# Optimization experiments

Hardware: AMD Instinct MI355X
Metric: run time of the kernel (lower is better)

## Reference

```python
import jax, jax.numpy as jnp
import numpy as np

N = 50000      # total nodes across batch of graphs
E = 800000     # total directed edges (avg degree 16)
B = 64         # number of graphs
D = 128        # input_dim == hidden_dim
L = 4          # num_layers - 1 GIN layers
OUT = 10
BN_EPS = 1e-5


def setup_inputs() -> dict:
    key = jax.random.key(0)
    ks = jax.random.split(key, 12)
    s = 0.05
    return {
        "x": jax.random.normal(ks[0], (N, D), jnp.float32),
        "pi": jax.random.uniform(ks[1], (B, 25), jnp.float32),
        "eps": jnp.zeros((L,), jnp.float32),
        "mlp_w1": jax.random.normal(ks[2], (L, D, D), jnp.float32) * s,
        "mlp_b1": jnp.zeros((L, D), jnp.float32),
        "mlp_bn_g": jnp.ones((L, D), jnp.float32),
        "mlp_bn_b": jnp.zeros((L, D), jnp.float32),
        "mlp_w2": jax.random.normal(ks[3], (L, D, D), jnp.float32) * s,
        "mlp_b2": jnp.zeros((L, D), jnp.float32),
        "bn_g": jnp.ones((L, D), jnp.float32),
        "bn_b": jnp.zeros((L, D), jnp.float32),
        "attend_w": jax.random.normal(ks[4], (D * (L + 1), 1), jnp.float32) * s,
        "attend_b": jnp.zeros((1,), jnp.float32),
        "pi_w": jax.random.normal(ks[5], (25, 16), jnp.float32) * s,
        "pi_b": jnp.zeros((16,), jnp.float32),
        "out_w": jax.random.normal(ks[6], (D * (L + 1) + 16, OUT), jnp.float32) * s,
        "out_b": jnp.zeros((OUT,), jnp.float32),
        "edge_index": jax.random.randint(ks[7], (2, E), 0, N, dtype=jnp.int32),
        "graph_id": jnp.sort(jax.random.randint(ks[8], (N,), 0, B, dtype=jnp.int32)),
    }


def _bn(z, g, b):
    # BatchNorm1d in training mode over all nodes (axis 0)
    m = z.mean(axis=0)
    v = z.var(axis=0)
    return (z - m) * jax.lax.rsqrt(v + BN_EPS) * g + b


def reference(x, pi, eps, mlp_w1, mlp_b1, mlp_bn_g, mlp_bn_b, mlp_w2, mlp_b2,
              bn_g, bn_b, attend_w, attend_b, pi_w, pi_b, out_w, out_b,
              edge_index, graph_id):
    src, dst = edge_index[0], edge_index[1]
    h = x
    reps = [x]
    for l in range(L):
        # GIN sum aggregation (learn_eps=True: no self-loops in Adj)
        pooled = jax.ops.segment_sum(h[src], dst, num_segments=N)
        pooled = pooled + (1.0 + eps[l]) * h
        # 2-layer MLP: Linear -> BN -> ReLU -> Linear
        z = jax.nn.relu(_bn(pooled @ mlp_w1[l] + mlp_b1[l], mlp_bn_g[l], mlp_bn_b[l]))
        z = z @ mlp_w2[l] + mlp_b2[l]
        # outer BN + ReLU
        h = jax.nn.relu(_bn(z, bn_g[l], bn_b[l]))
        reps.append(h)
    hr = jnp.concatenate(reps, axis=1)               # [N, D*(L+1)]
    # per-graph attention softmax over nodes
    scores = (hr @ attend_w + attend_b)[:, 0]        # [N]
    smax = jax.ops.segment_max(scores, graph_id, num_segments=B)
    e = jnp.exp(scores - smax[graph_id])
    denom = jax.ops.segment_sum(e, graph_id, num_segments=B)
    coef = e / denom[graph_id]
    gemb = jax.ops.segment_sum(hr * coef[:, None], graph_id, num_segments=B)  # [B, D*(L+1)]
    # persistence-image branch (PI computed host-side; treated as input)
    pie = jax.nn.relu(pi @ pi_w + pi_b)              # [B, 16]
    feat = jnp.concatenate([gemb, pie], axis=1)      # [B, D*(L+1)+16]
    return feat @ out_w + out_b                      # [B, OUT]
```

## Files before the change

### kernel.cpp

```cpp
#include <hip/hip_runtime.h>
#include <hip/hip_bf16.h>

#define NN 50000
#define EE 800000
#define BBG 64
#define DD 128
#define LLAY 4
#define HRW 640
#define NOUT 10
#define SCANB 196

typedef __hip_bfloat16 bf16;
typedef __attribute__((ext_vector_type(8))) short short8;
typedef __attribute__((ext_vector_type(4))) float f32x4;

__device__ __forceinline__ float b2f(bf16 v) { return __bfloat162float(v); }
__device__ __forceinline__ float bflo(unsigned u) { return __uint_as_float(u << 16); }
__device__ __forceinline__ float bfhi(unsigned u) { return __uint_as_float(u & 0xffff0000u); }
__device__ __forceinline__ unsigned short f2bs(float v) {
  bf16 h = __float2bfloat16(v);
  unsigned short r; __builtin_memcpy(&r, &h, 2); return r;
}
__device__ __forceinline__ int dtype_of(const void* __restrict__ bng) {
  return (*(const unsigned*)bng == 0x3F800000u) ? 1 : 0;
}
__device__ __forceinline__ float ldf(const void* __restrict__ p, long i, int dt) {
  return dt ? ((const float*)p)[i] : b2f(((const bf16*)p)[i]);
}

__device__ __forceinline__ int lower_bound_i(const int* __restrict__ a, int n, int key) {
  int lo = 0, hi = n;
  while (lo < hi) { int mid = (lo + hi) >> 1; if (a[mid] < key) lo = mid + 1; else hi = mid; }
  return lo;
}

__global__ __launch_bounds__(256) void gnn_init(const void* __restrict__ x,
                                                bf16* __restrict__ hrb,
                                                const void* __restrict__ w1,
                                                const void* __restrict__ w2,
                                                bf16* __restrict__ w1t,
                                                bf16* __restrict__ w2t,
                                                const void* __restrict__ aw,
                                                float* __restrict__ scores,
                                                const int* __restrict__ ei,
                                                int* __restrict__ counts,
                                                int* __restrict__ rel,
                                                const void* __restrict__ bng) {
  int dt = dtype_of(bng);
  int tid = threadIdx.x;
  if (blockIdx.x >= 6250) {
    int i = (blockIdx.x - 6250) * 256 + tid;
    int l = i >> 14, rem = i & 16383, n = rem >> 7, k = rem & 127;
    long src = (long)l * 16384 + k * 128 + n;
    w1t[i] = __float2bfloat16(ldf(w1, src, dt));
    w2t[i] = __float2bfloat16(ldf(w2, src, dt));
    return;
  }
  if (blockIdx.x >= 3125) {
    int e = (blockIdx.x - 3125) * 256 + tid;
    rel[e] = atomicAdd(&counts[ei[EE + e]], 1);
    return;
  }
  int n = blockIdx.x * 16 + (tid >> 4);
  int il = tid & 15;
  long base = (long)n * DD + il * 8;
  float v[8];
  if (dt) {
    float4 a0 = *(const float4*)((const float*)x + base);
    float4 a1 = *(const float4*)((const float*)x + base + 4);
    v[0] = a0.x; v[1] = a0.y; v[2] = a0.z; v[3] = a0.w;
    v[4] = a1.x; v[5] = a1.y; v[6] = a1.z; v[7] = a1.w;
  } else {
    uint4 u = *(const uint4*)((const bf16*)x + base);
    v[0] = bflo(u.x); v[1] = bfhi(u.x); v[2] = bflo(u.y); v[3] = bfhi(u.y);
    v[4] = bflo(u.z); v[5] = bfhi(u.z); v[6] = bflo(u.w); v[7] = bfhi(u.w);
  }
  uint4 o;
  o.x = (unsigned)f2bs(v[0]) | ((unsigned)f2bs(v[1]) << 16);
  o.y = (unsigned)f2bs(v[2]) | ((unsigned)f2bs(v[3]) << 16);
  o.z = (unsigned)f2bs(v[4]) | ((unsigned)f2bs(v[5]) << 16);
  o.w = (unsigned)f2bs(v[6]) | ((unsigned)f2bs(v[7]) << 16);
  *(uint4*)(hrb + (size_t)n * HRW + il * 8) = o;
  float ss = 0.f;
  #pragma unroll
  for (int k = 0; k < 8; k++) ss += v[k] * ldf(aw, il * 8 + k, dt);
  ss += __shfl_xor(ss, 1, 64); ss += __shfl_xor(ss, 2, 64);
  ss += __shfl_xor(ss, 4, 64); ss += __shfl_xor(ss, 8, 64);
  if (il == 0) unsafeAtomicAdd(&scores[n], ss);
}

__global__ __launch_bounds__(256) void gnn_scan1(const int* __restrict__ counts,
                                                 int* __restrict__ blocksum) {
  __shared__ int buf[256];
  int tid = threadIdx.x;
  int i = blockIdx.x * 256 + tid;
  buf[tid] = (i < NN) ? counts[i] : 0;
  __syncthreads();
  for (int s = 128; s > 0; s >>= 1) {
    if (tid < s) buf[tid] += buf[tid + s];
    __syncthreads();
  }
  if (tid == 0) blocksum[blockIdx.x] = buf[0];
}

__global__ __launch_bounds__(256) void gnn_scan3(const int* __restrict__ counts,
                                                 const int* __restrict__ blocksum,
                                                 int* __restrict__ rowstart) {
  __shared__ int buf[256];
  int tid = threadIdx.x;
  int partial = 0;
  for (int i = tid; i < blockIdx.x; i += 256) partial += blocksum[i];
  buf[tid] = partial;
  __syncthreads();
  for (int s = 128; s > 0; s >>= 1) {
    if (tid < s) buf[tid] += buf[tid + s];
    __syncthreads();
  }
  int offset = buf[0];
  __syncthreads();
  int i = blockIdx.x * 256 + tid;
  int v = (i < NN) ? counts[i] : 0;
  buf[tid] = v;
  __syncthreads();
  for (int ofs = 1; ofs < 256; ofs <<= 1) {
    int t = (tid >= ofs) ? buf[tid - ofs] : 0;
    __syncthreads();
    buf[tid] += t;
    __syncthreads();
  }
  int val = offset + buf[tid] - v;
  if (i < NN) rowstart[i] = val;
  if (blockIdx.x == SCANB - 1 && tid == 255) rowstart[NN] = offset + buf[255];
}

__global__ __launch_bounds__(256) void gnn_fill(const int* __restrict__ ei,
                                                const int* __restrict__ rowstart,
                                                const int* __restrict__ rel,
                                                int* __restrict__ csr_src) {
  int e = blockIdx.x * 256 + threadIdx.x;
  int src = ei[e];
  int dst = ei[EE + e];
  csr_src[rowstart[dst] + rel[e]] = src;
}

__device__ __forceinline__ void acc8(float* a, uint4 u) {
  a[0] += bflo(u.x); a[1] += bfhi(u.x);
  a[2] += bflo(u.y); a[3] += bfhi(u.y);
  a[4] += bflo(u.z); a[5] += bfhi(u.z);
  a[6] += bflo(u.w); a[7] += bfhi(u.w);
}

__device__ __forceinline__ float2 statsum(const float* __restrict__ stat, int c) {
  float s = 0.f, q = 0.f;
  #pragma unroll
  for (int k = 0; k < 8; k++) { s += stat[k * 256 + c]; q += stat[k * 256 + 128 + c]; }
  return make_float2(s, q);
}

__global__ __launch_bounds__(512) void gnn_gmg1(const bf16* __restrict__ hrb, int l,
                                                const int* __restrict__ rowstart,
                                                const int* __restrict__ csr_src,
                                                const void* __restrict__ eps,
                                                const bf16* __restrict__ Wt,
                                                const void* __restrict__ bias, int biasOfs,
                                                bf16* __restrict__ out,
                                                float* __restrict__ statOut,
                                                const void* __restrict__ bng) {
  int dt = dtype_of(bng);
  __shared__ __align__(16) unsigned ar[16][68];
  __shared__ int qhead;
  int tid = threadIdx.x, lane = tid & 63;
  int w = tid >> 6;
  int q = lane >> 4, il = lane & 15;
  int r0 = blockIdx.x * 16;
  const bf16* stripe = hrb + l * DD;
  float s = 1.0f + ldf(eps, l, dt);
  if (tid == 0) qhead = 0;
  __syncthreads();

  for (;;) {
    int i;
    if (lane == 0) i = atomicAdd(&qhead, 1);
    i = __shfl(i, 0, 64);
    if (i >= 16) break;
    int n = r0 + i;
    float a[8] = {0.f, 0.f, 0.f, 0.f, 0.f, 0.f, 0.f, 0.f};
    if (q == 0) {
      uint4 u = *(const uint4*)(stripe + (size_t)n * HRW + il * 8);
      a[0] = s * bflo(u.x); a[1] = s * bfhi(u.x);
      a[2] = s * bflo(u.y); a[3] = s * bfhi(u.y);
      a[4] = s * bflo(u.z); a[5] = s * bfhi(u.z);
      a[6] = s * bflo(u.w); a[7] = s * bfhi(u.w);
    }
    int start = rowstart[n], end = rowstart[n + 1];
    for (int base = start; base < end; base += 64) {
      int m = end - base; if (m > 64) m = 64;
      int idx = (base + lane < end) ? csr_src[base + lane] : 0;
      int j = 0;
      for (; j + 16 <= m; j += 16) {
        int s0 = __shfl(idx, j + q, 64);
        int s1 = __shfl(idx, j + 4 + q, 64);
        int s2 = __shfl(idx, j + 8 + q, 64);
        int s3 = __shfl(idx, j + 12 + q, 64);
        uint4 u0 = *(const uint4*)(stripe + (size_t)s0 * HRW + il * 8);
        uint4 u1 = *(const uint4*)(stripe + (size_t)s1 * HRW + il * 8);
        uint4 u2 = *(const uint4*)(stripe + (size_t)s2 * HRW + il * 8);
        uint4 u3 = *(const uint4*)(stripe + (size_t)s3 * HRW + il * 8);
        acc8(a, u0); acc8(a, u1); acc8(a, u2); acc8(a, u3);
      }
      for (; j + 8 <= m; j += 8) {
        int s0 = __shfl(idx, j + q, 64);
        int s1 = __shfl(idx, j + 4 + q, 64);
        uint4 u0 = *(const uint4*)(stripe + (size_t)s0 * HRW + il * 8);
        uint4 u1 = *(const uint4*)(stripe + (size_t)s1 * HRW + il * 8);
        acc8(a, u0); acc8(a, u1);
      }
      for (; j + 4 <= m; j += 4) {
        int src = __shfl(idx, j + q, 64);
        uint4 u = *(const uint4*)(stripe + (size_t)src * HRW + il * 8);
        acc8(a, u);
      }
      for (; j < m; j++) {
        int src = __shfl(idx, j, 64);
        if (q == 0) {
          uint4 u = *(const uint4*)(stripe + (size_t)src * HRW + il * 8);
          acc8(a, u);
        }
      }
    }
    #pragma unroll
    for (int k = 0; k < 8; k++) {
      a[k] += __shfl_xor(a[k], 16, 64);
      a[k] += __shfl_xor(a[k], 32, 64);
    }
    if (q == 0) {
      uint4 o;
      o.x = (unsigned)f2bs(a[0]) | ((unsigned)f2bs(a[1]) << 16);
      o.y = (unsigned)f2bs(a[2]) | ((unsigned)f2bs(a[3]) << 16);
      o.z = (unsigned)f2bs(a[4]) | ((unsigned)f2bs(a[5]) << 16);
      o.w = (unsigned)f2bs(a[6]) | ((unsigned)f2bs(a[7]) << 16);
      *(uint4*)&ar[i][il * 4] = o;
    }
  }
  __syncthreads();

  f32x4 acc = (f32x4){0.f, 0.f, 0.f, 0.f};
  #pragma unroll
  for (int ch = 0; ch < 4; ch++) {
    int k0 = ch * 32 + q * 8;
    uint4 raw = *(const uint4*)&ar[il][ch * 16 + q * 4];
    short8 af;
    __builtin_memcpy(&af, &raw, 16);
    short8 bfv = *(const short8*)(Wt + (w * 16 + il) * DD + k0);
    acc = __builtin_amdgcn_mfma_f32_16x16x32_bf16(af, bfv, acc, 0, 0, 0);
  }
  int col = w * 16 + il;
  float bv = ldf(bias, biasOfs + col, dt);
  float ss = 0.f, qq = 0.f;
  #pragma unroll
  for (int r = 0; r < 4; r++) {
    int row = r0 + q * 4 + r;
    float v = acc[r] + bv;
    out[(size_t)row * DD + col] = __float2bfloat16(v);
    ss += v; qq += v * v;
  }
  ss += __shfl_xor(ss, 16, 64);  ss += __shfl_xor(ss, 32, 64);
  qq += __shfl_xor(qq, 16, 64);  qq += __shfl_xor(qq, 32, 64);
  if (q == 0) {
    unsafeAtomicAdd(&statOut[(blockIdx.x & 7) * 256 + col], ss);
    unsafeAtomicAdd(&statOut[(blockIdx.x & 7) * 256 + 128 + col], qq);
  }
}

__global__ __launch_bounds__(256) void gnn_mgemm(const bf16* __restrict__ Abf,
                                                 const bf16* __restrict__ Wt,
                                                 const void* __restrict__ bias, int biasOfs,
                                                 bf16* __restrict__ out,
                                                 const float* __restrict__ statIn,
                                                 const void* __restrict__ g,
                                                 const void* __restrict__ bb, int parOfs,
                                                 float* __restrict__ statOut,
                                                 const void* __restrict__ bng) {
  int dt = dtype_of(bng);
  __shared__ float scf[128], shf[128];
  __shared__ float redS[4][128], redQ[4][128];
  int tid = threadIdx.x, w = tid >> 6, lane = tid & 63;
  int q = lane >> 4, il = lane & 15;
  if (tid < 128) {
    const float invN = 1.0f / NN;
    float2 sq = statsum(statIn, tid);
    float m = sq.x * invN;
    float rs = rsqrtf(sq.y * invN - m * m + 1e-5f);
    float gg = ldf(g, parOfs + tid, dt), bv = ldf(bb, parOfs + tid, dt);
    scf[tid] = rs * gg;
    shf[tid] = bv - m * rs * gg;
  }
  __syncthreads();
  int r0 = (blockIdx.x * 4 + w) * 16;
  int arow = r0 + il;
  int arowc = (arow < NN) ? arow : (NN - 1);
  f32x4 acc[8];
  #pragma unroll
  for (int i = 0; i < 8; i++) acc[i] = (f32x4){0.f, 0.f, 0.f, 0.f};
  #pragma unroll
  for (int ch = 0; ch < 4; ch++) {
    int k0 = ch * 32 + q * 8;
    uint4 raw = *(const uint4*)(Abf + (size_t)arowc * DD + k0);
    float4 c0 = *(const float4*)(scf + k0);
    float4 c1 = *(const float4*)(scf + k0 + 4);
    float4 d0 = *(const float4*)(shf + k0);
    float4 d1 = *(const float4*)(shf + k0 + 4);
    short8 af;
    af[0] = (short)f2bs(fmaxf(bflo(raw.x) * c0.x + d0.x, 0.f));
    af[1] = (short)f2bs(fmaxf(bfhi(raw.x) * c0.y + d0.y, 0.f));
    af[2] = (short)f2bs(fmaxf(bflo(raw.y) * c0.z + d0.z, 0.f));
    af[3] = (short)f2bs(fmaxf(bfhi(raw.y) * c0.w + d0.w, 0.f));
    af[4] = (short)f2bs(fmaxf(bflo(raw.z) * c1.x + d1.x, 0.f));
    af[5] = (short)f2bs(fmaxf(bfhi(raw.z) * c1.y + d1.y, 0.f));
    af[6] = (short)f2bs(fmaxf(bflo(raw.w) * c1.z + d1.z, 0.f));
    af[7] = (short)f2bs(fmaxf(bfhi(raw.w) * c1.w + d1.w, 0.f));
    #pragma unroll
    for (int ct = 0; ct < 8; ct++) {
      short8 bfv = *(const short8*)(Wt + (ct * 16 + il) * DD + k0);
      acc[ct] = __builtin_amdgcn_mfma_f32_16x16x32_bf16(af, bfv, acc[ct], 0, 0, 0);
    }
  }
  #pragma unroll
  for (int ct = 0; ct < 8; ct++) {
    int col = ct * 16 + il;
    float bv = ldf(bias, biasOfs + col, dt);
    float s = 0.f, qq = 0.f;
    #pragma unroll
    for (int r = 0; r < 4; r++) {
      int row = r0 + q * 4 + r;
      float v = acc[ct][r] + bv;
      if (row < NN) {
        out[(size_t)row * DD + col] = __float2bfloat16(v);
        s += v; qq += v * v;
      }
    }
    s += __shfl_xor(s, 16, 64);  s += __shfl_xor(s, 32, 64);
    qq += __shfl_xor(qq, 16, 64); qq += __shfl_xor(qq, 32, 64);
    if (q == 0) { redS[w][col] = s; redQ[w][col] = qq; }
  }
  __syncthreads();
  if (tid < 128) {
    float v = redS[0][tid] + redS[1][tid] + redS[2][tid] + redS[3][tid];
    unsafeAtomicAdd(&statOut[(blockIdx.x & 7) * 256 + tid], v);
  } else {
    int c = tid - 128;
    float v = redQ[0][c] + redQ[1][c] + redQ[2][c] + redQ[3][c];
    unsafeAtomicAdd(&statOut[(blockIdx.x & 7) * 256 + 128 + c], v);
  }
}

__global__ __launch_bounds__(256) void gnn_bn_relu(const bf16* __restrict__ z2,
                                                   const float* __restrict__ stat,
                                                   const void* __restrict__ g,
                                                   const void* __restrict__ bb, int parOfs,
                                                   bf16* __restrict__ hrb, int stripe,
                                                   const void* __restrict__ aw,
                                                   float* __restrict__ scores,
                                                   const void* __restrict__ bng) {
  int dt = dtype_of(bng);
  __shared__ float scf[128], shf[128], awf[128];
  int tid = threadIdx.x;
  if (tid < 128) {
    const float invN = 1.0f / NN;
    float2 sq = statsum(stat, tid);
    float m = sq.x * invN;
    float rs = rsqrtf(sq.y * invN - m * m + 1e-5f);
    float gg = ldf(g, parOfs + tid, dt), bv = ldf(bb, parOfs + tid, dt);
    scf[tid] = rs * gg;
    shf[tid] = bv - m * rs * gg;
    awf[tid] = ldf(aw, stripe * DD + tid, dt);
  }
  __syncthreads();
  int n = blockIdx.x * 16 + (tid >> 4);
  int il = tid & 15;
  int c0 = il * 8;
  uint4 u = *(const uint4*)(z2 + (size_t)n * DD + c0);
  float v[8];
  v[0] = bflo(u.x); v[1] = bfhi(u.x); v[2] = bflo(u.y); v[3] = bfhi(u.y);
  v[4] = bflo(u.z); v[5] = bfhi(u.z); v[6] = bflo(u.w); v[7] = bfhi(u.w);
  float ss = 0.f;
  #pragma unroll
  for (int k = 0; k < 8; k++) {
    v[k] = fmaxf(v[k] * scf[c0 + k] + shf[c0 + k], 0.f);
    ss += v[k] * awf[c0 + k];
  }
  uint4 o;
  o.x = (unsigned)f2bs(v[0]) | ((unsigned)f2bs(v[1]) << 16);
  o.y = (unsigned)f2bs(v[2]) | ((unsigned)f2bs(v[3]) << 16);
  o.z = (unsigned)f2bs(v[4]) | ((unsigned)f2bs(v[5]) << 16);
  o.w = (unsigned)f2bs(v[6]) | ((unsigned)f2bs(v[7]) << 16);
  *(uint4*)(hrb + (size_t)n * HRW + stripe * DD + c0) = o;
  ss += __shfl_xor(ss, 1, 64); ss += __shfl_xor(ss, 2, 64);
  ss += __shfl_xor(ss, 4, 64); ss += __shfl_xor(ss, 8, 64);
  if (il == 0) unsafeAtomicAdd(&scores[n], ss);
}

__global__ __launch_bounds__(128) void gnn_gemb(const bf16* __restrict__ hrb,
                                                const float* __restrict__ scores,
                                                const int* __restrict__ gid,
                                                float* __restrict__ gemb) {
  int b = blockIdx.x / 40;
  int part = blockIdx.x % 40;
  int chunk = part % 5;
  int slice = part / 5;
  int tid = threadIdx.x;
  int start = lower_bound_i(gid, NN, b);
  int end = lower_bound_i(gid, NN, b + 1);
  __shared__ float red[128];
  float mx = -3.4e38f;
  for (int n = start + tid; n < end; n += 128) mx = fmaxf(mx, scores[n]);
  red[tid] = mx;
  __syncthreads();
  for (int s = 64; s > 0; s >>= 1) {
    if (tid < s) red[tid] = fmaxf(red[tid], red[tid + s]);
    __syncthreads();
  }
  float smax = red[0];
  __syncthreads();
  float sum = 0.f;
  for (int n = start + tid; n < end; n += 128) sum += __expf(scores[n] - smax);
  red[tid] = sum;
  __syncthreads();
  for (int s = 64; s > 0; s >>= 1) {
    if (tid < s) red[tid] += red[tid + s];
    __syncthreads();
  }
  float denom = red[0];
  float inv = (denom > 0.f) ? 1.0f / denom : 0.f;
  int c = chunk * 128 + tid;
  float acc = 0.f;
  for (int n = start + slice; n < end; n += 8)
    acc += b2f(hrb[(size_t)n * HRW + c]) * __expf(scores[n] - smax) * inv;
  unsafeAtomicAdd(&gemb[b * HRW + c], acc);
}

__global__ __launch_bounds__(64) void gnn_final(const float* __restrict__ gemb,
                                                const void* __restrict__ pi,
                                                const void* __restrict__ piw,
                                                const void* __restrict__ pib,
                                                const void* __restrict__ ow,
                                                const void* __restrict__ ob,
                                                void* __restrict__ out,
                                                const void* __restrict__ bng) {
  int dt = dtype_of(bng);
  int b = blockIdx.x;
  int t = threadIdx.x;
  __shared__ float pie[16];
  if (t < 16) {
    float s = ldf(pib, t, dt);
    for (int i = 0; i < 25; i++) s += ldf(pi, b * 25 + i, dt) * ldf(piw, i * 16 + t, dt);
    pie[t] = fmaxf(s, 0.f);
  }
  __syncthreads();
  for (int o = 0; o < NOUT; o++) {
    float s = 0.f;
    for (int c = t; c < HRW + 16; c += 64) {
      float f = (c < HRW) ? gemb[b * HRW + c] : pie[c - HRW];
      s += f * ldf(ow, c * NOUT + o, dt);
    }
    #pragma unroll
    for (int m = 32; m > 0; m >>= 1) s += __shfl_xor(s, m, 64);
    if (t == 0) {
      float r = s + ldf(ob, o, dt);
      if (dt) ((float*)out)[b * NOUT + o] = r;
      else ((bf16*)out)[b * NOUT + o] = __float2bfloat16(r);
    }
  }
}

extern "C" void kernel_launch(void* const* d_in, const int* in_sizes, int n_in,
                              void* d_out, int out_size, void* d_ws, size_t ws_size,
                              hipStream_t stream) {
  const void* x    = d_in[0];
  const void* pi   = d_in[1];
  const void* eps  = d_in[2];
  const void* w1   = d_in[3];
  const void* b1   = d_in[4];
  const void* bng  = d_in[5];
  const void* bnb  = d_in[6];
  const void* w2   = d_in[7];
  const void* b2   = d_in[8];
  const void* obng = d_in[9];
  const void* obnb = d_in[10];
  const void* aw   = d_in[11];
  const void* piw  = d_in[13];
  const void* pib  = d_in[14];
  const void* ow   = d_in[15];
  const void* ob   = d_in[16];
  const int*  ei   = (const int*)d_in[17];
  const int*  gid  = (const int*)d_in[18];

  bf16*  hrb      = (bf16*)d_ws;
  bf16*  z1       = hrb + (size_t)NN * HRW;
  bf16*  z2       = z1 + (size_t)NN * DD;
  bf16*  w1t      = z2 + (size_t)NN * DD;
  bf16*  w2t      = w1t + LLAY * DD * DD;
  float* statbufs = (float*)(w2t + LLAY * DD * DD);
  float* gemb     = statbufs + 8 * 2048;
  int*   counts   = (int*)(gemb + BBG * HRW);
  float* scores   = (float*)(counts + NN);
  size_t zeroBytes = (size_t)(8 * 2048 + BBG * HRW + NN + NN) * 4;
  int*   rowstart = (int*)(scores + NN);
  int*   rel      = rowstart + NN + 1;
  int*   csr_src  = rel + EE;
  int*   blocksum = csr_src + EE;

  hipMemsetAsync(statbufs, 0, zeroBytes, stream);
  gnn_init<<<6506, 256, 0, stream>>>(x, hrb, w1, w2, w1t, w2t, aw, scores,
                                     ei, counts, rel, bng);

  gnn_scan1<<<SCANB, 256, 0, stream>>>(counts, blocksum);
  gnn_scan3<<<SCANB, 256, 0, stream>>>(counts, blocksum, rowstart);
  gnn_fill<<<EE / 256, 256, 0, stream>>>(ei, rowstart, rel, csr_src);

  for (int l = 0; l < LLAY; l++) {
    float* statA = statbufs + (l * 2 + 0) * 2048;
    float* statB = statbufs + (l * 2 + 1) * 2048;
    gnn_gmg1<<<NN / 16, 512, 0, stream>>>(hrb, l, rowstart, csr_src, eps,
                                          w1t + l * DD * DD, b1, l * DD,
                                          z1, statA, bng);
    gnn_mgemm<<<782, 256, 0, stream>>>(z1, w2t + l * DD * DD, b2, l * DD,
                                       z2, statA, bng, bnb, l * DD,
                                       statB, bng);
    gnn_bn_relu<<<NN / 16, 256, 0, stream>>>(z2, statB, obng, obnb, l * DD,
                                             hrb, l + 1, aw, scores, bng);
  }

  gnn_gemb<<<BBG * 40, 128, 0, stream>>>(hrb, scores, gid, gemb);
  gnn_final<<<BBG, 64, 0, stream>>>(gemb, pi, piw, pib, ow, ob, d_out, bng);
}
```

Measured before the change: 567.6 us.

## Use per-XCD counters and L2-scoped atomics instead of device-scope atomics

Degree counting now uses one counter array per XCD, read from the hardware XCC_ID register, with workgroup-scope atomics. The scan kernels combine these per-XCD counts and write per-XCD prefix offsets, which the CSR fill then uses. BN statistic accumulators are indexed by XCD and updated with raw global_atomic_add without system-scope semantics. Score accumulation changes from atomics to a plain store and read-modify-write, since each node has a single writer. The aim is to avoid costly cross-die coherent atomics, but correctness depends on workgroup-scope atomics being coherent within an XCD's L2.

Measured after the change: 556.4 us. 1.02x faster.

```diff
diff --git a/kernel.cpp b/kernel.cpp
--- a/kernel.cpp
+++ b/kernel.cpp
@@ -9,6 +9,7 @@
 #define HRW 640
 #define NOUT 10
 #define SCANB 196
+#define NXCD 8
 
 typedef __hip_bfloat16 bf16;
 typedef __attribute__((ext_vector_type(8))) short short8;
@@ -26,6 +27,16 @@
 }
 __device__ __forceinline__ float ldf(const void* __restrict__ p, long i, int dt) {
   return dt ? ((const float*)p)[i] : b2f(((const bf16*)p)[i]);
+}
+
+__device__ __forceinline__ int xccid() {
+  unsigned v;
+  asm("s_getreg_b32 %0, hwreg(HW_REG_XCC_ID)" : "=s"(v));
+  return (int)(v & (NXCD - 1));
+}
+
+__device__ __forceinline__ void fadd_l2(float* p, float v) {
+  asm volatile("global_atomic_add_f32 %0, %1, off" :: "v"(p), "v"(v) : "memory");
 }
 
 __device__ __forceinline__ int lower_bound_i(const int* __restrict__ a, int n, int key) {
@@ -43,7 +54,7 @@
                                                 const void* __restrict__ aw,
                                                 float* __restrict__ scores,
                                                 const int* __restrict__ ei,
-                                                int* __restrict__ counts,
+                                                int* __restrict__ cnt,
                                                 int* __restrict__ rel,
                                                 const void* __restrict__ bng) {
   int dt = dtype_of(bng);
@@ -58,7 +69,11 @@
   }
   if (blockIdx.x >= 3125) {
     int e = (blockIdx.x - 3125) * 256 + tid;
-    rel[e] = atomicAdd(&counts[ei[EE + e]], 1);
+    int dst = ei[EE + e];
+    int xid = xccid();
+    int old = __hip_atomic_fetch_add(&cnt[(size_t)xid * NN + dst], 1,
+                                     __ATOMIC_RELAXED, __HIP_MEMORY_SCOPE_WORKGROUP);
+    rel[e] = (xid << 24) | old;
     return;
   }
   int n = blockIdx.x * 16 + (tid >> 4);
@@ -86,15 +101,20 @@
   for (int k = 0; k < 8; k++) ss += v[k] * ldf(aw, il * 8 + k, dt);
   ss += __shfl_xor(ss, 1, 64); ss += __shfl_xor(ss, 2, 64);
   ss += __shfl_xor(ss, 4, 64); ss += __shfl_xor(ss, 8, 64);
-  if (il == 0) unsafeAtomicAdd(&scores[n], ss);
-}
-
-__global__ __launch_bounds__(256) void gnn_scan1(const int* __restrict__ counts,
+  if (il == 0) scores[n] = ss;
+}
+
+__global__ __launch_bounds__(256) void gnn_scan1(const int* __restrict__ cnt,
                                                  int* __restrict__ blocksum) {
   __shared__ int buf[256];
   int tid = threadIdx.x;
   int i = blockIdx.x * 256 + tid;
-  buf[tid] = (i < NN) ? counts[i] : 0;
+  int v = 0;
+  if (i < NN) {
+    #pragma unroll
+    for (int k = 0; k < NXCD; k++) v += cnt[(size_t)k * NN + i];
+  }
+  buf[tid] = v;
   __syncthreads();
   for (int s = 128; s > 0; s >>= 1) {
     if (tid < s) buf[tid] += buf[tid + s];
@@ -103,7 +123,7 @@
   if (tid == 0) blocksum[blockIdx.x] = buf[0];
 }
 
-__global__ __launch_bounds__(256) void gnn_scan3(const int* __restrict__ counts,
+__global__ __launch_bounds__(256) void gnn_scan3(int* __restrict__ cnt,
                                                  const int* __restrict__ blocksum,
                                                  int* __restrict__ rowstart) {
   __shared__ int buf[256];
@@ -119,7 +139,12 @@
   int offset = buf[0];
   __syncthreads();
   int i = blockIdx.x * 256 + tid;
-  int v = (i < NN) ? counts[i] : 0;
+  int c[NXCD];
+  int v = 0;
+  if (i < NN) {
+    #pragma unroll
+    for (int k = 0; k < NXCD; k++) { c[k] = cnt[(size_t)k * NN + i]; v += c[k]; }
+  }
   buf[tid] = v;
   __syncthreads();
   for (int ofs = 1; ofs < 256; ofs <<= 1) {
@@ -129,18 +154,26 @@
     __syncthreads();
   }
   int val = offset + buf[tid] - v;
-  if (i < NN) rowstart[i] = val;
+  if (i < NN) {
+    rowstart[i] = val;
+    int run = val;
+    #pragma unroll
+    for (int k = 0; k < NXCD; k++) { cnt[(size_t)k * NN + i] = run; run += c[k]; }
+  }
   if (blockIdx.x == SCANB - 1 && tid == 255) rowstart[NN] = offset + buf[255];
 }
 
 __global__ __launch_bounds__(256) void gnn_fill(const int* __restrict__ ei,
-                                                const int* __restrict__ rowstart,
+                                                const int* __restrict__ xcdpre,
                                                 const int* __restrict__ rel,
                                                 int* __restrict__ csr_src) {
   int e = blockIdx.x * 256 + threadIdx.x;
   int src = ei[e];
   int dst = ei[EE + e];
-  csr_src[rowstart[dst] + rel[e]] = src;
+  int r = rel[e];
+  int xid = r >> 24;
+  int rank = r & 0xFFFFFF;
+  csr_src[xcdpre[(size_t)xid * NN + dst] + rank] = src;
 }
 
 __device__ __forceinline__ void acc8(float* a, uint4 u) {
@@ -267,8 +300,9 @@
   ss += __shfl_xor(ss, 16, 64);  ss += __shfl_xor(ss, 32, 64);
   qq += __shfl_xor(qq, 16, 64);  qq += __shfl_xor(qq, 32, 64);
   if (q == 0) {
-    unsafeAtomicAdd(&statOut[(blockIdx.x & 7) * 256 + col], ss);
-    unsafeAtomicAdd(&statOut[(blockIdx.x & 7) * 256 + 128 + col], qq);
+    int xid = xccid();
+    fadd_l2(&statOut[xid * 256 + col], ss);
+    fadd_l2(&statOut[xid * 256 + 128 + col], qq);
   }
 }
 
@@ -344,13 +378,14 @@
     if (q == 0) { redS[w][col] = s; redQ[w][col] = qq; }
   }
   __syncthreads();
+  int xid = xccid();
   if (tid < 128) {
     float v = redS[0][tid] + redS[1][tid] + redS[2][tid] + redS[3][tid];
-    unsafeAtomicAdd(&statOut[(blockIdx.x & 7) * 256 + tid], v);
+    fadd_l2(&statOut[xid * 256 + tid], v);
   } else {
     int c = tid - 128;
     float v = redQ[0][c] + redQ[1][c] + redQ[2][c] + redQ[3][c];
-    unsafeAtomicAdd(&statOut[(blockIdx.x & 7) * 256 + 128 + c], v);
+    fadd_l2(&statOut[xid * 256 + 128 + c], v);
   }
 }
 
@@ -397,7 +432,7 @@
   *(uint4*)(hrb + (size_t)n * HRW + stripe * DD + c0) = o;
   ss += __shfl_xor(ss, 1, 64); ss += __shfl_xor(ss, 2, 64);
   ss += __shfl_xor(ss, 4, 64); ss += __shfl_xor(ss, 8, 64);
-  if (il == 0) unsafeAtomicAdd(&scores[n], ss);
+  if (il == 0) scores[n] += ss;
 }
 
 __global__ __launch_bounds__(128) void gnn_gemb(const bf16* __restrict__ hrb,
@@ -502,9 +537,9 @@
   bf16*  w2t      = w1t + LLAY * DD * DD;
   float* statbufs = (float*)(w2t + LLAY * DD * DD);
   float* gemb     = statbufs + 8 * 2048;
-  int*   counts   = (int*)(gemb + BBG * HRW);
-  float* scores   = (float*)(counts + NN);
-  size_t zeroBytes = (size_t)(8 * 2048 + BBG * HRW + NN + NN) * 4;
+  int*   cnt      = (int*)(gemb + BBG * HRW);
+  size_t zeroBytes = (size_t)(8 * 2048 + BBG * HRW + NXCD * NN) * 4;
+  float* scores   = (float*)(cnt + (size_t)NXCD * NN);
   int*   rowstart = (int*)(scores + NN);
   int*   rel      = rowstart + NN + 1;
   int*   csr_src  = rel + EE;
@@ -512,11 +547,11 @@
 
   hipMemsetAsync(statbufs, 0, zeroBytes, stream);
   gnn_init<<<6506, 256, 0, stream>>>(x, hrb, w1, w2, w1t, w2t, aw, scores,
-                                     ei, counts, rel, bng);
-
-  gnn_scan1<<<SCANB, 256, 0, stream>>>(counts, blocksum);
-  gnn_scan3<<<SCANB, 256, 0, stream>>>(counts, blocksum, rowstart);
-  gnn_fill<<<EE / 256, 256, 0, stream>>>(ei, rowstart, rel, csr_src);
+                                     ei, cnt, rel, bng);
+
+  gnn_scan1<<<SCANB, 256, 0, stream>>>(cnt, blocksum);
+  gnn_scan3<<<SCANB, 256, 0, stream>>>(cnt, blocksum, rowstart);
+  gnn_fill<<<EE / 256, 256, 0, stream>>>(ei, cnt, rel, csr_src);
 
   for (int l = 0; l < LLAY; l++) {
     float* statA = statbufs + (l * 2 + 0) * 2048;
```
